# Kernel optimization log

Measured on AMD Instinct MI355X. Metric: run time of the kernel, lower is better.

Reference implementation:

```python
import math
import jax, jax.numpy as jnp
import numpy as np

HIDDEN = 1024   # config.hidden_size
INTER = 4096    # config.intermediate_size
EXPERTS = 8     # config.moe_experts == config.global_experts
B, T = 4, 2048
EPS = 1e-12     # config.epsilon
CAP_FACTOR = 1.0
MIN_CAP = 4


def layer_norm(x, g, b, eps=EPS):
    m = jnp.mean(x, axis=-1, keepdims=True)
    v = jnp.var(x, axis=-1, keepdims=True)
    return (x - m) * jax.lax.rsqrt(v + eps) * g + b


def top1_gate(x, wg, capacity):
    # DeepSpeed top1gating: softmax gate, argmax expert, capacity-based token drop.
    logits = x @ wg                                    # [S, E]
    gates = jax.nn.softmax(logits, axis=-1)
    E = wg.shape[-1]
    idx = jnp.argmax(gates, axis=-1)                   # [S]
    mask1 = jax.nn.one_hot(idx, E, dtype=gates.dtype)  # [S, E]
    locations = jnp.cumsum(mask1, axis=0) - mask1      # exclusive cumsum = slot within expert
    mask1 = mask1 * (locations < capacity).astype(gates.dtype)  # drop overflow tokens
    gates1_s = jnp.sum(gates * mask1, axis=-1)         # [S] prob of chosen expert
    loc_s = jnp.sum(locations * mask1, axis=-1).astype(jnp.int32)
    loc_oh = jax.nn.one_hot(loc_s, capacity, dtype=gates.dtype)          # [S, C]
    combine = gates1_s[:, None, None] * mask1[:, :, None] * loc_oh[:, None, :]  # [S, E, C]
    dispatch = jax.lax.stop_gradient((combine > 0).astype(x.dtype))      # bool mask in torch
    return combine, dispatch


def setup_inputs() -> dict:
    key = jax.random.key(0)
    ks = jax.random.split(key, 8)
    s = 0.02
    return {
        "x": jax.random.normal(ks[0], (B, T, HIDDEN), jnp.float32),
        "attn_nw": jnp.ones((HIDDEN,), jnp.float32),
        "attn_nb": jnp.zeros((HIDDEN,), jnp.float32),
        "wg": jax.random.normal(ks[1], (HIDDEN, EXPERTS), jnp.float32) * s,
        "inter_w": jax.random.normal(ks[2], (EXPERTS, HIDDEN, INTER), jnp.float32) * s,
        "inter_b": jnp.zeros((EXPERTS, INTER), jnp.float32),
        "output_w": jax.random.normal(ks[3], (EXPERTS, INTER, HIDDEN), jnp.float32) * s,
        "output_b": jnp.zeros((EXPERTS, HIDDEN), jnp.float32),
        "res_inter_w": jax.random.normal(ks[4], (HIDDEN, INTER), jnp.float32) * s,
        "res_inter_b": jnp.zeros((INTER,), jnp.float32),
        "res_output_w": jax.random.normal(ks[5], (INTER, HIDDEN), jnp.float32) * s,
        "res_output_b": jnp.zeros((HIDDEN,), jnp.float32),
        "res_coef": jax.random.normal(ks[6], (HIDDEN, 2), jnp.float32) * s,
    }


def reference(x, attn_nw, attn_nb, wg, inter_w, inter_b, output_w, output_b,
              res_inter_w, res_inter_b, res_output_w, res_output_b, res_coef):
    Bx, Tx, M = x.shape
    S = Bx * Tx
    E = wg.shape[-1]
    capacity = max(MIN_CAP, math.ceil(S / E * CAP_FACTOR))  # static

    residual = x.reshape(S, M)                  # attention output + bias (attention = identity here)
    attn_out = layer_norm(residual, attn_nw, attn_nb)  # ds_layernorm

    # gate + dispatch: einsum_sec_sm_ecm
    combine, dispatch = top1_gate(attn_out, wg, capacity)
    dispatched = jnp.einsum('sec,sm->ecm', dispatch, attn_out)  # [E, C, M]

    # expert MLPs: fused gemm-gelu then output projection + bias
    h = jax.nn.gelu(jnp.einsum('ecm,emi->eci', dispatched, inter_w) + inter_b[:, None, :], approximate=True)
    expert_out = jnp.einsum('eci,eim->ecm', h, output_w) + output_b[:, None, :]

    # gated combine: matmul(combine.reshape(S, E*C), expert_out.reshape(E*C, M))
    moe_out = jnp.einsum('sec,ecm->sm', combine, expert_out)

    # residual-MLP branch (mlp_type == 'residual')
    rh = jax.nn.gelu(attn_out @ res_inter_w + res_inter_b, approximate=True)
    res_mlp_out = rh @ res_output_w + res_output_b
    coef = jax.nn.softmax(attn_out @ res_coef, axis=-1)          # [S, 2]
    out = res_mlp_out * coef[:, :1] + moe_out * coef[:, 1:]      # moe_res_matmul

    out = out + residual                                         # bias_residual
    return out.reshape(Bx, Tx, M)
```

## Files before the change

### kernel.cpp

```cpp
#include <hip/hip_runtime.h>
#include <hip/hip_bf16.h>
#include <type_traits>

#define S_TOK 8192
#define HID 1024
#define INTERX 4096
#define NEXP 8
#define CAPX 1024
#define MTOT 16384

using f32x4 = __attribute__((ext_vector_type(4))) float;
using bf16x8 = __attribute__((ext_vector_type(8))) short;

__device__ __forceinline__ short f2bf(float f) {
    union { float f; unsigned u; } v; v.f = f;
    unsigned r = (v.u + 0x7FFFu + ((v.u >> 16) & 1u)) >> 16;
    return (short)r;
}
__device__ __forceinline__ float bflo(int p) {
    union { unsigned u; float f; } v; v.u = (unsigned)p << 16; return v.f;
}
__device__ __forceinline__ float bfhi(int p) {
    union { unsigned u; float f; } v; v.u = (unsigned)p & 0xffff0000u; return v.f;
}

__device__ __forceinline__ float gelu_f(float x) {
    float x2 = x * x;
    float t = __expf(x * fmaf(x2, -0.07135677f, -1.5957691f));
    return x * __builtin_amdgcn_rcpf(1.0f + t);
}

__device__ __forceinline__ void gl_lds16(const short* g, short* l) {
    __builtin_amdgcn_global_load_lds(
        (const __attribute__((address_space(1))) void*)g,
        (__attribute__((address_space(3))) void*)l, 16, 0, 0);
}

template<int PERM>
__global__ __launch_bounds__(256) void convtrans_kernel(
    const float* __restrict__ src_e, const float* __restrict__ src_r,
    short* __restrict__ dst, int K, int N, long sSrc, long sDst)
{
    __shared__ __align__(16) short tile[64][72];
    long z = blockIdx.z;
    const float* s = (z < 8) ? (src_e + z * sSrc) : src_r;
    short* d = dst + z * sDst;
    int n0 = blockIdx.x * 64, k0 = blockIdx.y * 64;
    int t = threadIdx.x;
    int br = t >> 4, bc = t & 15;
    const float* sp = s + (long)(k0 + br * 4) * N + n0 + bc * 4;
    float4 r0 = *(const float4*)(sp);
    float4 r1 = *(const float4*)(sp + N);
    float4 r2 = *(const float4*)(sp + 2 * (long)N);
    float4 r3 = *(const float4*)(sp + 3 * (long)N);
    if (PERM) {
        float rr[4][4] = { {r0.x,r0.y,r0.z,r0.w}, {r1.x,r1.y,r1.z,r1.w},
                           {r2.x,r2.y,r2.z,r2.w}, {r3.x,r3.y,r3.z,r3.w} };
#pragma unroll
        for (int j = 0; j < 4; j++) {
            int kl = br * 4 + j;
            int kp = (kl & 15) * 4 + (kl >> 4);
#pragma unroll
            for (int q = 0; q < 4; q++)
                tile[bc * 4 + q][kp] = f2bf(rr[j][q]);
        }
    } else {
        short4 c0 = { f2bf(r0.x), f2bf(r1.x), f2bf(r2.x), f2bf(r3.x) };
        short4 c1 = { f2bf(r0.y), f2bf(r1.y), f2bf(r2.y), f2bf(r3.y) };
        short4 c2 = { f2bf(r0.z), f2bf(r1.z), f2bf(r2.z), f2bf(r3.z) };
        short4 c3 = { f2bf(r0.w), f2bf(r1.w), f2bf(r2.w), f2bf(r3.w) };
        *(short4*)&tile[bc * 4 + 0][br * 4] = c0;
        *(short4*)&tile[bc * 4 + 1][br * 4] = c1;
        *(short4*)&tile[bc * 4 + 2][br * 4] = c2;
        *(short4*)&tile[bc * 4 + 3][br * 4] = c3;
    }
    __syncthreads();
    int n = t >> 2, kc = (t & 3) * 16;
    int4 o0 = *(const int4*)&tile[n][kc];
    int4 o1 = *(const int4*)&tile[n][kc + 8];
    short* dp = d + (long)(n0 + n) * K + k0 + kc;
    *(int4*)(dp) = o0;
    *(int4*)(dp + 8) = o1;
}

__global__ __launch_bounds__(256) void ln_gate_kernel(
    const float* __restrict__ x, const float* __restrict__ nw, const float* __restrict__ nb,
    const float* __restrict__ wg, const float* __restrict__ rcf,
    short* __restrict__ attn_bf, int* __restrict__ eidx, float* __restrict__ gate,
    float* __restrict__ coef0, float* __restrict__ coef1,
    int* __restrict__ map2, int* __restrict__ zbufi)
{
    int s = blockIdx.x, tid = threadIdx.x;
    int lane = tid & 63, wave = tid >> 6;
    __shared__ float wred[4][2];
    __shared__ double gred[4][10];

    if (tid == 0) {
        map2[s] = -1;
        map2[NEXP * CAPX + s] = s;
    }
    if (s == 0) ((int2*)zbufi)[tid] = int2{0, 0};

    float4 xv = *(const float4*)(x + (size_t)s * HID + tid * 4);
    float sum = xv.x + xv.y + xv.z + xv.w;
    float sq  = xv.x*xv.x + xv.y*xv.y + xv.z*xv.z + xv.w*xv.w;
#pragma unroll
    for (int o = 32; o > 0; o >>= 1) {
        sum += __shfl_down(sum, o, 64);
        sq  += __shfl_down(sq, o, 64);
    }
    if (lane == 0) { wred[wave][0] = sum; wred[wave][1] = sq; }
    __syncthreads();
    float ts = wred[0][0] + wred[1][0] + wred[2][0] + wred[3][0];
    float tq = wred[0][1] + wred[1][1] + wred[2][1] + wred[3][1];
    float m  = ts * (1.0f / HID);
    float var = tq * (1.0f / HID) - m * m;
    float rs = rsqrtf(var + 1e-12f);

    float4 g4 = *(const float4*)(nw + tid * 4);
    float4 b4 = *(const float4*)(nb + tid * 4);
    float y[4];
    y[0] = (xv.x - m) * rs * g4.x + b4.x;
    y[1] = (xv.y - m) * rs * g4.y + b4.y;
    y[2] = (xv.z - m) * rs * g4.z + b4.z;
    y[3] = (xv.w - m) * rs * g4.w + b4.w;

    short4 yb = { f2bf(y[0]), f2bf(y[1]), f2bf(y[2]), f2bf(y[3]) };
    *(short4*)(attn_bf + (size_t)s * HID + tid * 4) = yb;

    double a[10];
#pragma unroll
    for (int q = 0; q < 10; q++) a[q] = 0.0;
#pragma unroll
    for (int j = 0; j < 4; j++) {
        int k = tid * 4 + j;
        float4 w0 = *(const float4*)(wg + k * 8);
        float4 w1 = *(const float4*)(wg + k * 8 + 4);
        double yj = (double)y[j];
        a[0] += yj * w0.x; a[1] += yj * w0.y; a[2] += yj * w0.z; a[3] += yj * w0.w;
        a[4] += yj * w1.x; a[5] += yj * w1.y; a[6] += yj * w1.z; a[7] += yj * w1.w;
        float2 rc = *(const float2*)(rcf + k * 2);
        a[8] += yj * rc.x; a[9] += yj * rc.y;
    }
#pragma unroll
    for (int o = 32; o > 0; o >>= 1)
#pragma unroll
        for (int q = 0; q < 10; q++) a[q] += __shfl_down(a[q], o, 64);
    if (lane == 0)
#pragma unroll
        for (int q = 0; q < 10; q++) gred[wave][q] = a[q];
    __syncthreads();
    if (tid == 0) {
        float l[8];
#pragma unroll
        for (int e = 0; e < 8; e++)
            l[e] = (float)(gred[0][e] + gred[1][e] + gred[2][e] + gred[3][e]);
        int bi = 0; float bv = l[0];
#pragma unroll
        for (int e = 1; e < 8; e++) if (l[e] > bv) { bv = l[e]; bi = e; }
        float den = 0.0f;
#pragma unroll
        for (int e = 0; e < 8; e++) den += expf(l[e] - bv);
        gate[s] = 1.0f / den;
        eidx[s] = bi;
        float r0 = (float)(gred[0][8] + gred[1][8] + gred[2][8] + gred[3][8]);
        float r1 = (float)(gred[0][9] + gred[1][9] + gred[2][9] + gred[3][9]);
        float mx = fmaxf(r0, r1);
        float e0 = expf(r0 - mx), e1 = expf(r1 - mx);
        float inv = 1.0f / (e0 + e1);
        coef0[s] = e0 * inv; coef1[s] = e1 * inv;
    }
}

__global__ __launch_bounds__(256) void assign_kernel(
    const int* __restrict__ eidx, int* __restrict__ slot, int* __restrict__ map2)
{
    int tid = threadIdx.x;
    __shared__ int cnt[2][256][NEXP];
    int c[NEXP];
#pragma unroll
    for (int e = 0; e < NEXP; e++) c[e] = 0;
    int base = tid * 32;
    for (int t = 0; t < 32; t++) { int e = eidx[base + t]; c[e]++; }
#pragma unroll
    for (int e = 0; e < NEXP; e++) cnt[0][tid][e] = c[e];
    __syncthreads();

    int src = 0;
    for (int step = 1; step < 256; step <<= 1) {
        int dst = src ^ 1;
#pragma unroll
        for (int e = 0; e < NEXP; e++) {
            int v = cnt[src][tid][e];
            if (tid >= step) v += cnt[src][tid - step][e];
            cnt[dst][tid][e] = v;
        }
        __syncthreads();
        src = dst;
    }
    int off[NEXP];
#pragma unroll
    for (int e = 0; e < NEXP; e++) off[e] = (tid > 0) ? cnt[src][tid - 1][e] : 0;
    for (int t = 0; t < 32; t++) {
        int s = base + t;
        int e = eidx[s];
        int loc = off[e]++;
        if (loc < CAPX) { slot[s] = loc; map2[e * CAPX + loc] = s; }
        else            { slot[s] = -1; }
    }
}

template<int EPI, int GATHER>
__global__ __launch_bounds__(256, 2) void gemm_kernel(
    const short* __restrict__ A, const short* __restrict__ W,
    const float* __restrict__ bias_e, const float* __restrict__ bias_r,
    short* __restrict__ out, const int* __restrict__ map2,
    const short* __restrict__ zbuf, int N, int K, long sW, long sB)
{
    __shared__ __align__(16) short a_lds[128 * 64];
    __shared__ __align__(16) short b_lds[256 * 64];

    int L = blockIdx.x + gridDim.x * blockIdx.y;
    int by = (L & 7) * 16 + ((L >> 3) & 15);
    int bx = L >> 7;

    long e = by >> 3; if (e > 8) e = 8;
    const short* Wb = W + e * sW;
    const float* biasb = (by < 64) ? (bias_e + e * sB) : bias_r;

    int tid = threadIdx.x;
    int lane = tid & 63, wave = tid >> 6;
    int wm = wave & 1, wn = wave >> 1;
    int lm = lane & 15, lq = lane >> 4;
    int lr = lane >> 3, ch = lane & 7;
    int chs = (ch ^ lr) * 8;

    const short* pA[4];
    const short* pB[8];
#pragma unroll
    for (int it = 0; it < 4; it++) {
        int row = (wave * 4 + it) * 8 + lr;
        if (GATHER) {
            int s = map2[by * 128 + row];
            pA[it] = (s >= 0) ? (A + (long)s * K) : zbuf;
        } else {
            pA[it] = A + ((long)by * 128 + row) * K;
        }
    }
#pragma unroll
    for (int it = 0; it < 8; it++) {
        int row = (wave * 8 + it) * 8 + lr;
        pB[it] = Wb + ((long)bx * 256 + row) * K;
    }

    f32x4 acc[4][8];
#pragma unroll
    for (int i = 0; i < 4; i++)
#pragma unroll
        for (int j = 0; j < 8; j++) acc[i][j] = { 0.f, 0.f, 0.f, 0.f };

    for (int kb = 0; kb < K; kb += 64) {
#pragma unroll
        for (int it = 0; it < 4; it++)
            gl_lds16(pA[it] + kb + chs, a_lds + (wave * 4 + it) * 512);
#pragma unroll
        for (int it = 0; it < 8; it++)
            gl_lds16(pB[it] + kb + chs, b_lds + (wave * 8 + it) * 512);
        __syncthreads();
#pragma unroll
        for (int ks = 0; ks < 64; ks += 32) {
            int po = ((lq ^ (lm & 7)) * 8) ^ ks;
            bf16x8 af[4], bfr[8];
#pragma unroll
            for (int i = 0; i < 4; i++)
                af[i] = *(const bf16x8*)(a_lds + (wm * 64 + i * 16 + lm) * 64 + po);
#pragma unroll
            for (int j = 0; j < 8; j++)
                bfr[j] = *(const bf16x8*)(b_lds + (wn * 128 + j * 16 + lm) * 64 + po);
#pragma unroll
            for (int i = 0; i < 4; i++)
#pragma unroll
                for (int j = 0; j < 8; j++)
                    acc[i][j] = __builtin_amdgcn_mfma_f32_16x16x32_bf16(af[i], bfr[j], acc[i][j], 0, 0, 0);
        }
        __syncthreads();
    }

    float bb[8];
#pragma unroll
    for (int j = 0; j < 8; j++)
        bb[j] = biasb[bx * 256 + wn * 128 + j * 16 + lm];

#pragma unroll
    for (int i = 0; i < 4; i++) {
#pragma unroll
        for (int r = 0; r < 4; r++) {
            long row = (long)by * 128 + wm * 64 + i * 16 + lq * 4 + r;
            if (EPI == 1) {
                short* rp = out + row * N + bx * 256 + wn * 128;
#pragma unroll
                for (int h = 0; h < 2; h++) {
                    int b0 = f2bf(gelu_f(acc[i][h*4+0][r] + bb[h*4+0]));
                    int b1 = f2bf(gelu_f(acc[i][h*4+1][r] + bb[h*4+1]));
                    int b2 = f2bf(gelu_f(acc[i][h*4+2][r] + bb[h*4+2]));
                    int b3 = f2bf(gelu_f(acc[i][h*4+3][r] + bb[h*4+3]));
                    int2 pk;
                    pk.x = (b0 & 0xFFFF) | (b1 << 16);
                    pk.y = (b2 & 0xFFFF) | (b3 << 16);
                    *(int2*)(rp + h * 64 + lm * 4) = pk;
                }
            } else {
#pragma unroll
                for (int j = 0; j < 8; j++) {
                    int col = bx * 256 + wn * 128 + j * 16 + lm;
                    out[row * N + col] = f2bf(acc[i][j][r] + bb[j]);
                }
            }
        }
    }
}

__global__ __launch_bounds__(256) void final_kernel(
    const float* __restrict__ x, const short* __restrict__ eout2,
    const int* __restrict__ eidx, const int* __restrict__ slot,
    const float* __restrict__ gate, const float* __restrict__ coef0,
    const float* __restrict__ coef1, float* __restrict__ out)
{
    int s = blockIdx.x, tid = threadIdx.x;
    float c0 = coef0[s], g = gate[s] * coef1[s];
    int sl = slot[s], e = eidx[s];
    float4 xv = *(const float4*)(x + (size_t)s * HID + tid * 4);
    int2 rm = *(const int2*)(eout2 + ((size_t)(NEXP * CAPX + s)) * HID + tid * 4);
    int2 mo = { 0, 0 };
    if (sl >= 0) mo = *(const int2*)(eout2 + ((size_t)(e * CAPX + sl)) * HID + tid * 4);
    float4 o;
    o.x = bflo(rm.x) * c0 + g * bflo(mo.x) + xv.x;
    o.y = bfhi(rm.x) * c0 + g * bfhi(mo.x) + xv.y;
    o.z = bflo(rm.y) * c0 + g * bflo(mo.y) + xv.z;
    o.w = bfhi(rm.y) * c0 + g * bfhi(mo.y) + xv.w;
    *(float4*)(out + (size_t)s * HID + tid * 4) = o;
}

extern "C" void kernel_launch(void* const* d_in, const int* in_sizes, int n_in,
                              void* d_out, int out_size, void* d_ws, size_t ws_size,
                              hipStream_t stream) {
    const float* x           = (const float*)d_in[0];
    const float* attn_nw     = (const float*)d_in[1];
    const float* attn_nb     = (const float*)d_in[2];
    const float* wg          = (const float*)d_in[3];
    const float* inter_w     = (const float*)d_in[4];
    const float* inter_b     = (const float*)d_in[5];
    const float* output_w    = (const float*)d_in[6];
    const float* output_b    = (const float*)d_in[7];
    const float* res_inter_w = (const float*)d_in[8];
    const float* res_inter_b = (const float*)d_in[9];
    const float* res_output_w= (const float*)d_in[10];
    const float* res_output_b= (const float*)d_in[11];
    const float* res_coef    = (const float*)d_in[12];
    float* out = (float*)d_out;

    char* ws = (char*)d_ws;
    size_t off = 0;
    auto alloc = [&](size_t bytes) { void* p = ws + off; off += (bytes + 255) & ~(size_t)255; return p; };
    char* region1 = (char*)alloc((size_t)MTOT * HID * 2);
    short* wreg   = (short*)alloc((size_t)9 * HID * INTERX * 2);
    short* hbuf2  = (short*)alloc((size_t)MTOT * INTERX * 2);
    int*   eidx   = (int*)alloc(S_TOK * 4);
    int*   slot   = (int*)alloc(S_TOK * 4);
    float* gate   = (float*)alloc(S_TOK * 4);
    float* c0     = (float*)alloc(S_TOK * 4);
    float* c1     = (float*)alloc(S_TOK * 4);
    int*   map2   = (int*)alloc(MTOT * 4);
    short* zbuf   = (short*)alloc(1024 * 2);

    short* attn_bf = (short*)region1;
    short* eout2   = (short*)region1;
    short* w1t = wreg;
    short* w2t = wreg;

    convtrans_kernel<0><<<dim3(INTERX/64, HID/64, 9), 256, 0, stream>>>(
        inter_w, res_inter_w, w1t, HID, INTERX, (long)HID*INTERX, (long)HID*INTERX);

    ln_gate_kernel<<<S_TOK, 256, 0, stream>>>(x, attn_nw, attn_nb, wg, res_coef,
                                              attn_bf, eidx, gate, c0, c1,
                                              map2, (int*)zbuf);
    assign_kernel<<<1, 256, 0, stream>>>(eidx, slot, map2);

    gemm_kernel<1, 1><<<dim3(INTERX/256, 128), 256, 0, stream>>>(
        attn_bf, w1t, inter_b, res_inter_b, hbuf2, map2, zbuf,
        INTERX, HID, (long)HID*INTERX, INTERX);

    convtrans_kernel<1><<<dim3(HID/64, INTERX/64, 9), 256, 0, stream>>>(
        output_w, res_output_w, w2t, INTERX, HID, (long)INTERX*HID, (long)INTERX*HID);

    gemm_kernel<0, 0><<<dim3(HID/256, 128), 256, 0, stream>>>(
        hbuf2, w2t, output_b, res_output_b, eout2, nullptr, zbuf,
        HID, INTERX, (long)INTERX*HID, HID);

    final_kernel<<<S_TOK, 256, 0, stream>>>(x, eout2, eidx, slot, gate, c0, c1, out);

    (void)in_sizes; (void)n_in; (void)out_size; (void)ws_size;
}
```

Measured before the change: 733.7 us.

## Rewrite MoE GEMM as 256x256 tile, 8-wave, double-buffered pipelined kernel

Replaces the 128x256-tile, 4-wave GEMM with a 256x256-tile kernel using 8 waves and a 128 KB double-buffered LDS. Global-to-LDS staging for the next K tiles is interleaved with MFMA work on quadrants of the current tile, using explicit barriers, waitcnts and setprio. The aim is to hide load latency and improve operand reuse, at the cost of much larger LDS use, which may cap occupancy at one block per CU, plus fragile hand-tuned synchronization.

Result: faster. 713.3 us (-2.8%).

```diff
diff --git a/kernel.cpp b/kernel.cpp
--- a/kernel.cpp
+++ b/kernel.cpp
@@ -211,22 +211,21 @@
 }
 
 template<int EPI, int GATHER>
-__global__ __launch_bounds__(256, 2) void gemm_kernel(
+__global__ __launch_bounds__(512, 2) void gemm8_kernel(
     const short* __restrict__ A, const short* __restrict__ W,
     const float* __restrict__ bias_e, const float* __restrict__ bias_r,
     short* __restrict__ out, const int* __restrict__ map2,
     const short* __restrict__ zbuf, int N, int K, long sW, long sB)
 {
-    __shared__ __align__(16) short a_lds[128 * 64];
-    __shared__ __align__(16) short b_lds[256 * 64];
-
-    int L = blockIdx.x + gridDim.x * blockIdx.y;
-    int by = (L & 7) * 16 + ((L >> 3) & 15);
-    int bx = L >> 7;
-
-    long e = by >> 3; if (e > 8) e = 8;
+    __shared__ __align__(16) short lds[65536];
+
+    int L = blockIdx.x;
+    int by = (L & 7) * 8 + ((L >> 3) & 7);
+    int bx = L >> 6;
+
+    long e = by >> 2; if (e > 8) e = 8;
     const short* Wb = W + e * sW;
-    const float* biasb = (by < 64) ? (bias_e + e * sB) : bias_r;
+    const float* biasb = (by < 32) ? (bias_e + e * sB) : bias_r;
 
     int tid = threadIdx.x;
     int lane = tid & 63, wave = tid >> 6;
@@ -234,85 +233,142 @@
     int lm = lane & 15, lq = lane >> 4;
     int lr = lane >> 3, ch = lane & 7;
     int chs = (ch ^ lr) * 8;
+    int po0 = (lq ^ (lm & 7)) * 8;
+    int po1 = po0 ^ 32;
 
     const short* pA[4];
-    const short* pB[8];
-#pragma unroll
-    for (int it = 0; it < 4; it++) {
-        int row = (wave * 4 + it) * 8 + lr;
-        if (GATHER) {
-            int s = map2[by * 128 + row];
-            pA[it] = (s >= 0) ? (A + (long)s * K) : zbuf;
-        } else {
-            pA[it] = A + ((long)by * 128 + row) * K;
-        }
-    }
-#pragma unroll
-    for (int it = 0; it < 8; it++) {
-        int row = (wave * 8 + it) * 8 + lr;
-        pB[it] = Wb + ((long)bx * 256 + row) * K;
-    }
-
-    f32x4 acc[4][8];
-#pragma unroll
-    for (int i = 0; i < 4; i++)
-#pragma unroll
-        for (int j = 0; j < 8; j++) acc[i][j] = { 0.f, 0.f, 0.f, 0.f };
-
-    for (int kb = 0; kb < K; kb += 64) {
-#pragma unroll
-        for (int it = 0; it < 4; it++)
-            gl_lds16(pA[it] + kb + chs, a_lds + (wave * 4 + it) * 512);
-#pragma unroll
-        for (int it = 0; it < 8; it++)
-            gl_lds16(pB[it] + kb + chs, b_lds + (wave * 8 + it) * 512);
-        __syncthreads();
-#pragma unroll
-        for (int ks = 0; ks < 64; ks += 32) {
-            int po = ((lq ^ (lm & 7)) * 8) ^ ks;
-            bf16x8 af[4], bfr[8];
-#pragma unroll
-            for (int i = 0; i < 4; i++)
-                af[i] = *(const bf16x8*)(a_lds + (wm * 64 + i * 16 + lm) * 64 + po);
-#pragma unroll
-            for (int j = 0; j < 8; j++)
-                bfr[j] = *(const bf16x8*)(b_lds + (wn * 128 + j * 16 + lm) * 64 + po);
-#pragma unroll
-            for (int i = 0; i < 4; i++)
-#pragma unroll
-                for (int j = 0; j < 8; j++)
-                    acc[i][j] = __builtin_amdgcn_mfma_f32_16x16x32_bf16(af[i], bfr[j], acc[i][j], 0, 0, 0);
-        }
-        __syncthreads();
-    }
-
-    float bb[8];
-#pragma unroll
-    for (int j = 0; j < 8; j++)
-        bb[j] = biasb[bx * 256 + wn * 128 + j * 16 + lm];
-
-#pragma unroll
-    for (int i = 0; i < 4; i++) {
+    const short* pAb = nullptr;
+    if (GATHER) {
+#pragma unroll
+        for (int h = 0; h < 2; h++)
+#pragma unroll
+            for (int it = 0; it < 2; it++) {
+                int rt = h * 128 + (wave * 2 + it) * 8 + lr;
+                int s = map2[by * 256 + rt];
+                pA[h * 2 + it] = ((s >= 0) ? (A + (long)s * K) : zbuf) + chs;
+            }
+    } else {
+        pAb = A + ((long)by * 256 + wave * 16 + lr) * K + chs;
+    }
+    const short* pBb = Wb + ((long)bx * 256 + wave * 16 + lr) * K + chs;
+
+#define A_SRC(h,it,t) (GATHER ? (pA[(h)*2+(it)] + (t)*64) \
+                              : (pAb + ((h)*128 + (it)*8)*(long)K + (t)*64))
+#define B_SRC(h,it,t) (pBb + ((h)*128 + (it)*8)*(long)K + (t)*64)
+#define STAGE_A(b,h,t) do { \
+    gl_lds16(A_SRC(h,0,t), lds + (b)*32768 + (h)*8192 + wave*1024); \
+    gl_lds16(A_SRC(h,1,t), lds + (b)*32768 + (h)*8192 + wave*1024 + 512); } while (0)
+#define STAGE_B(b,h,t) do { \
+    gl_lds16(B_SRC(h,0,t), lds + (b)*32768 + 16384 + (h)*8192 + wave*1024); \
+    gl_lds16(B_SRC(h,1,t), lds + (b)*32768 + 16384 + (h)*8192 + wave*1024 + 512); } while (0)
+#define LOAD_A(QM) do { _Pragma("unroll") \
+    for (int i2 = 0; i2 < 4; i2++) { \
+        const short* ap = base + (QM)*8192 + wm*4096 + i2*1024 + lm*64; \
+        af[i2][0] = *(const bf16x8*)(ap + po0); \
+        af[i2][1] = *(const bf16x8*)(ap + po1); } } while (0)
+#define LOAD_B(QN,DST) do { _Pragma("unroll") \
+    for (int j2 = 0; j2 < 2; j2++) { \
+        const short* bp = base + 16384 + (QN)*8192 + wn*2048 + j2*1024 + lm*64; \
+        DST[j2][0] = *(const bf16x8*)(bp + po0); \
+        DST[j2][1] = *(const bf16x8*)(bp + po1); } } while (0)
+#define MFMA_Q(QM,QN,BSRC) do { _Pragma("unroll") \
+    for (int i2 = 0; i2 < 4; i2++) { _Pragma("unroll") \
+    for (int j2 = 0; j2 < 2; j2++) { \
+        f32x4 t0 = acc[(QM)*4+i2][(QN)*2+j2]; \
+        t0 = __builtin_amdgcn_mfma_f32_16x16x32_bf16(af[i2][0], BSRC[j2][0], t0, 0, 0, 0); \
+        t0 = __builtin_amdgcn_mfma_f32_16x16x32_bf16(af[i2][1], BSRC[j2][1], t0, 0, 0, 0); \
+        acc[(QM)*4+i2][(QN)*2+j2] = t0; } } } while (0)
+#define SYNC_IN do { \
+    __builtin_amdgcn_sched_barrier(0); \
+    __builtin_amdgcn_s_barrier(); \
+    asm volatile("s_waitcnt lgkmcnt(0)" ::: "memory"); \
+    __builtin_amdgcn_sched_barrier(0); \
+    __builtin_amdgcn_s_setprio(1); } while (0)
+#define SYNC_OUT do { \
+    __builtin_amdgcn_s_setprio(0); \
+    __builtin_amdgcn_sched_barrier(0); \
+    __builtin_amdgcn_s_barrier(); \
+    __builtin_amdgcn_sched_barrier(0); } while (0)
+
+    f32x4 acc[8][4];
+#pragma unroll
+    for (int i = 0; i < 8; i++)
+#pragma unroll
+        for (int j = 0; j < 4; j++) acc[i][j] = { 0.f, 0.f, 0.f, 0.f };
+
+    const int NT = K >> 6;
+
+    STAGE_A(0, 0, 0); STAGE_B(0, 0, 0);
+    STAGE_A(0, 1, 0); STAGE_B(0, 1, 0);
+    STAGE_A(1, 0, 1); STAGE_B(1, 0, 1);
+    __builtin_amdgcn_sched_barrier(0);
+    asm volatile("s_waitcnt vmcnt(4)" ::: "memory");
+    __builtin_amdgcn_s_barrier();
+    __builtin_amdgcn_sched_barrier(0);
+
+    bf16x8 af[4][2], b0v[2][2], b1v[2][2];
+
+    for (int tt = 0; tt < NT; ++tt) {
+        const int cur = tt & 1, nxt = cur ^ 1;
+        const bool s1 = (tt + 1 < NT), s2 = (tt + 2 < NT);
+        const short* base = lds + cur * 32768;
+
+        LOAD_A(0); LOAD_B(0, b0v);
+        if (s1) STAGE_A(nxt, 1, tt + 1);
+        SYNC_IN;  MFMA_Q(0, 0, b0v);  SYNC_OUT;
+
+        LOAD_B(1, b1v);
+        if (s1) STAGE_B(nxt, 1, tt + 1);
+        SYNC_IN;  MFMA_Q(0, 1, b1v);  SYNC_OUT;
+
+        LOAD_A(1);
+        if (s2) STAGE_A(cur, 0, tt + 2);
+        SYNC_IN;  MFMA_Q(1, 0, b0v);  SYNC_OUT;
+
+        if (s2) STAGE_B(cur, 0, tt + 2);
+        SYNC_IN;  MFMA_Q(1, 1, b1v);
+        __builtin_amdgcn_s_setprio(0);
+        __builtin_amdgcn_sched_barrier(0);
+        if (s2)      { asm volatile("s_waitcnt vmcnt(4)" ::: "memory"); }
+        else if (s1) { asm volatile("s_waitcnt vmcnt(0)" ::: "memory"); }
+        __builtin_amdgcn_s_barrier();
+        __builtin_amdgcn_sched_barrier(0);
+    }
+
+#undef A_SRC
+#undef B_SRC
+#undef STAGE_A
+#undef STAGE_B
+#undef LOAD_A
+#undef LOAD_B
+#undef MFMA_Q
+#undef SYNC_IN
+#undef SYNC_OUT
+
+    float bb[4];
+#pragma unroll
+    for (int j = 0; j < 4; j++)
+        bb[j] = biasb[bx * 256 + (j >> 1) * 128 + wn * 32 + (j & 1) * 16 + lm];
+
+#pragma unroll
+    for (int i = 0; i < 8; i++) {
+        long rowb = (long)by * 256 + (i >> 2) * 128 + wm * 64 + (i & 3) * 16 + lq * 4;
 #pragma unroll
         for (int r = 0; r < 4; r++) {
-            long row = (long)by * 128 + wm * 64 + i * 16 + lq * 4 + r;
+            long row = rowb + r;
             if (EPI == 1) {
-                short* rp = out + row * N + bx * 256 + wn * 128;
-#pragma unroll
-                for (int h = 0; h < 2; h++) {
-                    int b0 = f2bf(gelu_f(acc[i][h*4+0][r] + bb[h*4+0]));
-                    int b1 = f2bf(gelu_f(acc[i][h*4+1][r] + bb[h*4+1]));
-                    int b2 = f2bf(gelu_f(acc[i][h*4+2][r] + bb[h*4+2]));
-                    int b3 = f2bf(gelu_f(acc[i][h*4+3][r] + bb[h*4+3]));
-                    int2 pk;
-                    pk.x = (b0 & 0xFFFF) | (b1 << 16);
-                    pk.y = (b2 & 0xFFFF) | (b3 << 16);
-                    *(int2*)(rp + h * 64 + lm * 4) = pk;
+                short* rp = out + row * N + bx * 256;
+#pragma unroll
+                for (int jj = 0; jj < 2; jj++) {
+                    int b0 = f2bf(gelu_f(acc[i][jj * 2 + 0][r] + bb[jj * 2 + 0]));
+                    int b1 = f2bf(gelu_f(acc[i][jj * 2 + 1][r] + bb[jj * 2 + 1]));
+                    int pk = (b0 & 0xFFFF) | (b1 << 16);
+                    *(int*)(rp + (jj * 2 + (wn >> 1)) * 64 + lm * 4 + (wn & 1) * 2) = pk;
                 }
             } else {
 #pragma unroll
-                for (int j = 0; j < 8; j++) {
-                    int col = bx * 256 + wn * 128 + j * 16 + lm;
+                for (int j = 0; j < 4; j++) {
+                    int col = bx * 256 + (j >> 1) * 128 + wn * 32 + (j & 1) * 16 + lm;
                     out[row * N + col] = f2bf(acc[i][j][r] + bb[j]);
                 }
             }
@@ -386,14 +442,14 @@
                                               map2, (int*)zbuf);
     assign_kernel<<<1, 256, 0, stream>>>(eidx, slot, map2);
 
-    gemm_kernel<1, 1><<<dim3(INTERX/256, 128), 256, 0, stream>>>(
+    gemm8_kernel<1, 1><<<dim3((MTOT/256) * (INTERX/256)), 512, 0, stream>>>(
         attn_bf, w1t, inter_b, res_inter_b, hbuf2, map2, zbuf,
         INTERX, HID, (long)HID*INTERX, INTERX);
 
     convtrans_kernel<1><<<dim3(HID/64, INTERX/64, 9), 256, 0, stream>>>(
         output_w, res_output_w, w2t, INTERX, HID, (long)INTERX*HID, (long)INTERX*HID);
 
-    gemm_kernel<0, 0><<<dim3(HID/256, 128), 256, 0, stream>>>(
+    gemm8_kernel<0, 0><<<dim3((MTOT/256) * (HID/256)), 512, 0, stream>>>(
         hbuf2, w2t, output_b, res_output_b, eout2, nullptr, zbuf,
         HID, INTERX, (long)INTERX*HID, HID);
 
```
